# Optimization experiments

Measured on AMD Instinct MI355X. Metric: run time of the kernel, lower is better.

The kernel has to match this reference:

```python
import jax, jax.numpy as jnp
import numpy as np

B, C, NNEG, D = 4096, 5, 20, 128
NUM_EMB = 400000  # vocab * num_poly


def setup_inputs() -> dict:
    key = jax.random.key(0)
    k1, k2, k3, k4, k5 = jax.random.split(key, 5)
    iword = jax.random.randint(k1, (B,), 0, NUM_EMB, dtype=jnp.int64)
    owords = jax.random.randint(k2, (B, C), 0, NUM_EMB, dtype=jnp.int64)
    nwords = jax.random.randint(k3, (B, C * NNEG), 0, NUM_EMB, dtype=jnp.int64)
    emb1 = jax.random.normal(k4, (NUM_EMB, D), dtype=jnp.float32) * 0.1
    emb2 = jax.random.normal(k5, (NUM_EMB, D), dtype=jnp.float32) * 0.1
    return {"iword": iword, "owords": owords, "nwords": nwords,
            "emb1": emb1, "emb2": emb2}


def reference(iword, owords, nwords, emb1, emb2):
    v1 = emb1[iword]          # [B, D] center vectors
    v2 = emb2[owords]         # [B, C, D] context vectors
    vn = emb2[nwords]         # [B, C*NNEG, D] negative vectors
    # positive: mean over context of log sigmoid(v2 . v1)
    o_scores = jnp.einsum('bcd,bd->bc', v2, v1)
    oloss = jax.nn.log_sigmoid(o_scores).mean(axis=1)              # [B]
    # negatives: vectors are negated -> log sigmoid(-score), sum over negs, mean over context
    n_scores = jnp.einsum('bkd,bd->bk', vn, v1)                    # [B, C*NNEG]
    nloss = jax.nn.log_sigmoid(-n_scores).reshape(-1, C, NNEG).sum(axis=2).mean(axis=1)  # [B]
    return -(oloss + nloss).mean()
```

## Files before the change

kernel.cpp:

```cpp
#include <hip/hip_runtime.h>
#include <math.h>

#define B 4096
#define C 5
#define NNEG 20
#define D 128
#define NROWS (C + C * NNEG)

__device__ __forceinline__ float log_sigmoid(float x) {
    return fminf(x, 0.0f) - log1pf(__expf(-fabsf(x)));
}

__global__ __launch_bounds__(256) void sgns_partial(
    const int* __restrict__ iword,
    const int* __restrict__ owords,
    const int* __restrict__ nwords,
    const float* __restrict__ emb1,
    const float* __restrict__ emb2,
    float* __restrict__ partial)
{
    const int b    = blockIdx.x;
    const int tid  = threadIdx.x;
    const int lane = tid & 63;
    const int wave = tid >> 6;
    const int grp  = lane >> 3;
    const int j    = lane & 7;
    const int base = wave * 8 + grp;

    const long center = (long)iword[b] * D;
    const float4* v1p = (const float4*)(emb1 + center);
    float4 v1f[4];
    #pragma unroll
    for (int k = 0; k < 4; ++k) v1f[k] = v1p[j + 8 * k];

    int   rIdx[4];
    float sgn[4];
    bool  valid[4];
    #pragma unroll
    for (int p = 0; p < 4; ++p) {
        const int r = base + 32 * p;
        valid[p] = (r < NROWS);
        const int rr = valid[p] ? r : 0;
        const bool pos = (rr < C);
        sgn[p] = pos ? 1.0f : -1.0f;
        rIdx[p] = pos ? owords[b * C + rr]
                      : nwords[b * (C * NNEG) + (rr - C)];
    }

    float4 rw[4][4];
    #pragma unroll
    for (int p = 0; p < 4; ++p) {
        const float4* rp = (const float4*)(emb2 + (long)rIdx[p] * D);
        #pragma unroll
        for (int k = 0; k < 4; ++k) rw[p][k] = rp[j + 8 * k];
    }

    float acc = 0.0f;
    #pragma unroll
    for (int p = 0; p < 4; ++p) {
        float s = 0.0f;
        #pragma unroll
        for (int k = 0; k < 4; ++k) {
            s += v1f[k].x * rw[p][k].x + v1f[k].y * rw[p][k].y
               + v1f[k].z * rw[p][k].z + v1f[k].w * rw[p][k].w;
        }
        s += __shfl_xor(s, 1, 64);
        s += __shfl_xor(s, 2, 64);
        s += __shfl_xor(s, 4, 64);

        const float v = log_sigmoid(sgn[p] * s);
        acc += valid[p] ? v : 0.0f;
    }

    acc += __shfl_xor(acc, 8, 64);
    acc += __shfl_xor(acc, 16, 64);
    acc += __shfl_xor(acc, 32, 64);

    __shared__ float wsum[4];
    if (lane == 0) wsum[wave] = acc;
    __syncthreads();
    if (tid == 0)
        partial[b] = wsum[0] + wsum[1] + wsum[2] + wsum[3];
}

__global__ __launch_bounds__(256) void sgns_reduce(
    const float* __restrict__ partial,
    float* __restrict__ out)
{
    const int tid = threadIdx.x;
    float acc = 0.0f;
    for (int i = tid; i < B; i += 256) acc += partial[i];

    #pragma unroll
    for (int off = 32; off > 0; off >>= 1)
        acc += __shfl_xor(acc, off, 64);

    __shared__ float ws[4];
    if ((tid & 63) == 0) ws[tid >> 6] = acc;
    __syncthreads();
    if (tid == 0) out[0] = -(ws[0] + ws[1] + ws[2] + ws[3]) / (float)(B * C);
}

extern "C" void kernel_launch(void* const* d_in, const int* in_sizes, int n_in,
                              void* d_out, int out_size, void* d_ws, size_t ws_size,
                              hipStream_t stream) {
    const int*   iword  = (const int*)d_in[0];
    const int*   owords = (const int*)d_in[1];
    const int*   nwords = (const int*)d_in[2];
    const float* emb1   = (const float*)d_in[3];
    const float* emb2   = (const float*)d_in[4];
    float* out     = (float*)d_out;
    float* partial = (float*)d_ws;

    sgns_partial<<<B, 256, 0, stream>>>(iword, owords, nwords, emb1, emb2, partial);
    sgns_reduce<<<1, 256, 0, stream>>>(partial, out);
}
```

Measured before the change: 355.8 us.

## Process four batch rows per block with prefetched indices for the next row

Each block now handles four consecutive batch rows in a loop instead of one, cutting the grid to 1024 blocks. The index loads for the next row are issued before the current row's dot products, so their latency overlaps compute. It also skips the invalid fourth row load instead of masking it, and adds launch bounds with a minimum of four blocks. The cost is fewer blocks in flight on a gather-bound kernel, which can reduce memory-level parallelism, plus a per-iteration barrier.

```diff
diff --git a/kernel.cpp b/kernel.cpp
--- a/kernel.cpp
+++ b/kernel.cpp
@@ -6,12 +6,34 @@
 #define NNEG 20
 #define D 128
 #define NROWS (C + C * NNEG)
+#define PER 4
+#define NBLK (B / PER)
 
 __device__ __forceinline__ float log_sigmoid(float x) {
     return fminf(x, 0.0f) - log1pf(__expf(-fabsf(x)));
 }
 
-__global__ __launch_bounds__(256) void sgns_partial(
+__device__ __forceinline__ int fetch_idx(const int* __restrict__ ow,
+                                         const int* __restrict__ nw,
+                                         int b, int r) {
+    return (r < C) ? ow[b * C + r] : nw[b * (C * NNEG) + (r - C)];
+}
+
+__device__ __forceinline__ float row_term(const float4 v1f[4], const float4 rwp[4],
+                                          float sgn) {
+    float s = 0.0f;
+    #pragma unroll
+    for (int k = 0; k < 4; ++k) {
+        s += v1f[k].x * rwp[k].x + v1f[k].y * rwp[k].y
+           + v1f[k].z * rwp[k].z + v1f[k].w * rwp[k].w;
+    }
+    s += __shfl_xor(s, 1, 64);
+    s += __shfl_xor(s, 2, 64);
+    s += __shfl_xor(s, 4, 64);
+    return log_sigmoid(sgn * s);
+}
+
+__global__ __launch_bounds__(256, 4) void sgns_partial(
     const int* __restrict__ iword,
     const int* __restrict__ owords,
     const int* __restrict__ nwords,
@@ -19,68 +41,76 @@
     const float* __restrict__ emb2,
     float* __restrict__ partial)
 {
-    const int b    = blockIdx.x;
     const int tid  = threadIdx.x;
     const int lane = tid & 63;
     const int wave = tid >> 6;
     const int grp  = lane >> 3;
     const int j    = lane & 7;
     const int base = wave * 8 + grp;
+    const bool valid3 = (base + 96) < NROWS;
+    const float sgn0 = (base < C) ? 1.0f : -1.0f;
 
-    const long center = (long)iword[b] * D;
-    const float4* v1p = (const float4*)(emb1 + center);
-    float4 v1f[4];
+    __shared__ float wsum[2][4];
+
+    const int b0 = blockIdx.x * PER;
+    int centerN = iword[b0];
+    int idxN[4];
     #pragma unroll
-    for (int k = 0; k < 4; ++k) v1f[k] = v1p[j + 8 * k];
+    for (int p = 0; p < 3; ++p)
+        idxN[p] = fetch_idx(owords, nwords, b0, base + 32 * p);
+    idxN[3] = valid3 ? fetch_idx(owords, nwords, b0, base + 96) : 0;
 
-    int   rIdx[4];
-    float sgn[4];
-    bool  valid[4];
-    #pragma unroll
-    for (int p = 0; p < 4; ++p) {
-        const int r = base + 32 * p;
-        valid[p] = (r < NROWS);
-        const int rr = valid[p] ? r : 0;
-        const bool pos = (rr < C);
-        sgn[p] = pos ? 1.0f : -1.0f;
-        rIdx[p] = pos ? owords[b * C + rr]
-                      : nwords[b * (C * NNEG) + (rr - C)];
+    for (int it = 0; it < PER; ++it) {
+        const int b = b0 + it;
+        const int centerC = centerN;
+        int idxC[4];
+        #pragma unroll
+        for (int p = 0; p < 4; ++p) idxC[p] = idxN[p];
+
+        const float4* v1p = (const float4*)(emb1 + (long)centerC * D);
+        float4 v1f[4];
+        #pragma unroll
+        for (int k = 0; k < 4; ++k) v1f[k] = v1p[j + 8 * k];
+
+        float4 rw[4][4];
+        #pragma unroll
+        for (int p = 0; p < 3; ++p) {
+            const float4* rp = (const float4*)(emb2 + (long)idxC[p] * D);
+            #pragma unroll
+            for (int k = 0; k < 4; ++k) rw[p][k] = rp[j + 8 * k];
+        }
+        if (valid3) {
+            const float4* rp = (const float4*)(emb2 + (long)idxC[3] * D);
+            #pragma unroll
+            for (int k = 0; k < 4; ++k) rw[3][k] = rp[j + 8 * k];
+        }
+
+        if (it + 1 < PER) {
+            const int bn = b + 1;
+            centerN = iword[bn];
+            #pragma unroll
+            for (int p = 0; p < 3; ++p)
+                idxN[p] = fetch_idx(owords, nwords, bn, base + 32 * p);
+            idxN[3] = valid3 ? fetch_idx(owords, nwords, bn, base + 96) : 0;
+        }
+
+        float acc = 0.0f;
+        acc += row_term(v1f, rw[0], sgn0);
+        acc += row_term(v1f, rw[1], -1.0f);
+        acc += row_term(v1f, rw[2], -1.0f);
+        if (valid3)
+            acc += row_term(v1f, rw[3], -1.0f);
+
+        acc += __shfl_xor(acc, 8, 64);
+        acc += __shfl_xor(acc, 16, 64);
+        acc += __shfl_xor(acc, 32, 64);
+
+        if (lane == 0) wsum[it & 1][wave] = acc;
+        __syncthreads();
+        if (tid == 0)
+            partial[b] = wsum[it & 1][0] + wsum[it & 1][1]
+                       + wsum[it & 1][2] + wsum[it & 1][3];
     }
-
-    float4 rw[4][4];
-    #pragma unroll
-    for (int p = 0; p < 4; ++p) {
-        const float4* rp = (const float4*)(emb2 + (long)rIdx[p] * D);
-        #pragma unroll
-        for (int k = 0; k < 4; ++k) rw[p][k] = rp[j + 8 * k];
-    }
-
-    float acc = 0.0f;
-    #pragma unroll
-    for (int p = 0; p < 4; ++p) {
-        float s = 0.0f;
-        #pragma unroll
-        for (int k = 0; k < 4; ++k) {
-            s += v1f[k].x * rw[p][k].x + v1f[k].y * rw[p][k].y
-               + v1f[k].z * rw[p][k].z + v1f[k].w * rw[p][k].w;
-        }
-        s += __shfl_xor(s, 1, 64);
-        s += __shfl_xor(s, 2, 64);
-        s += __shfl_xor(s, 4, 64);
-
-        const float v = log_sigmoid(sgn[p] * s);
-        acc += valid[p] ? v : 0.0f;
-    }
-
-    acc += __shfl_xor(acc, 8, 64);
-    acc += __shfl_xor(acc, 16, 64);
-    acc += __shfl_xor(acc, 32, 64);
-
-    __shared__ float wsum[4];
-    if (lane == 0) wsum[wave] = acc;
-    __syncthreads();
-    if (tid == 0)
-        partial[b] = wsum[0] + wsum[1] + wsum[2] + wsum[3];
 }
 
 __global__ __launch_bounds__(256) void sgns_reduce(
@@ -112,6 +142,6 @@
     float* out     = (float*)d_out;
     float* partial = (float*)d_ws;
 
-    sgns_partial<<<B, 256, 0, stream>>>(iword, owords, nwords, emb1, emb2, partial);
+    sgns_partial<<<NBLK, 256, 0, stream>>>(iword, owords, nwords, emb1, emb2, partial);
     sgns_reduce<<<1, 256, 0, stream>>>(partial, out);
 }
```

Result: no change. 357.2 us (+0.4%).
